# Performance work log

Measured on AMD Instinct MI355X. Metric: run time of the kernel, lower is better.

The kernel has to match this reference:

```python
import jax, jax.numpy as jnp
import numpy as np

B_, N, C = 4096, 49, 384
H = 12
HD = C // H
NW = 64
SCALE = HD ** -0.5


def setup_inputs() -> dict:
    key = jax.random.key(0)
    k_x, k_m, k_w1, k_b1, k_w2, k_b2 = jax.random.split(key, 6)
    x = jax.random.normal(k_x, (B_, N, C), dtype=jnp.float32)
    # shifted-window style additive mask: 0 = allowed, -100 = blocked
    mask = jnp.where(jax.random.uniform(k_m, (NW, N, N)) < 0.5, 0.0, -100.0).astype(jnp.float32)
    w_qkv = jax.random.normal(k_w1, (3 * C, C), dtype=jnp.float32) * (C ** -0.5)
    b_qkv = jax.random.normal(k_b1, (3 * C,), dtype=jnp.float32) * 0.02
    w_proj = jax.random.normal(k_w2, (C, C), dtype=jnp.float32) * (C ** -0.5)
    b_proj = jax.random.normal(k_b2, (C,), dtype=jnp.float32) * 0.02
    return {"x": x, "mask": mask, "w_qkv": w_qkv, "b_qkv": b_qkv,
            "w_proj": w_proj, "b_proj": b_proj}


def reference(x, mask, w_qkv, b_qkv, w_proj, b_proj):
    # qkv projection: (B_, N, 3C)
    qkv = x @ w_qkv.T + b_qkv
    qkv = qkv.reshape(B_, N, 3, H, HD).transpose(2, 0, 3, 1, 4)  # (3, B_, H, N, HD)
    q, k, v = qkv[0], qkv[1], qkv[2]
    q = q * SCALE
    attn = jnp.einsum('bhnd,bhmd->bhnm', q, k)  # (B_, H, N, N)
    # additive shifted-window mask, per-window pattern broadcast over batch & heads
    attn = attn.reshape(B_ // NW, NW, H, N, N) + mask[None, :, None]
    attn = attn.reshape(B_, H, N, N)
    attn = jax.nn.softmax(attn, axis=-1)
    out = jnp.einsum('bhnm,bhmd->bhnd', attn, v)  # (B_, H, N, HD)
    out = out.transpose(0, 2, 1, 3).reshape(B_, N, C)
    return out @ w_proj.T + b_proj
```

## Files before the change

kernel.cpp:

```cpp
#include <hip/hip_runtime.h>
#include <cstdio>
#include <cstdint>


typedef __attribute__((ext_vector_type(8))) short bfrag8;
typedef __attribute__((ext_vector_type(4))) float facc4;
typedef __attribute__((ext_vector_type(16))) float facc16;

#define SCALE_Q 0.17677669529663687f
#define PLANE 6422528ull

__device__ __forceinline__ unsigned short f2bf(float f) {
  unsigned int x = __float_as_uint(f);
  x += 0x7fffu + ((x >> 16) & 1u);
  return (unsigned short)(x >> 16);
}

__device__ __forceinline__ void gload_lds16(const void* g, void* l) {
  __builtin_amdgcn_global_load_lds(
      (const __attribute__((address_space(1))) unsigned int*)g,
      (__attribute__((address_space(3))) unsigned int*)l,
      16, 0, 0);
}

__global__ void __launch_bounds__(256) cvt_bf16_kernel(const float* __restrict__ src,
                                                       unsigned short* __restrict__ dst) {
  size_t i = ((size_t)blockIdx.x * 256u + threadIdx.x) * 4u;
  const float4 v = *(const float4*)(src + i);
  ushort4 o;
  o.x = f2bf(v.x); o.y = f2bf(v.y); o.z = f2bf(v.z); o.w = f2bf(v.w);
  *(ushort4*)(dst + i) = o;
}

__global__ void __launch_bounds__(256) mask_bits_kernel(
    const float* __restrict__ mask, unsigned long long* __restrict__ bits) {
  const int idx = blockIdx.x * 256 + threadIdx.x;
  const int wdw = idx >> 6, m = idx & 63;
  unsigned long long bm = 0ull;
  if (m < 49) {
    const float* mp = mask + (size_t)wdw * 2401 + (size_t)m * 49;
    for (int n = 0; n < 49; ++n)
      if (mp[n] > -50.f) bm |= (1ull << n);
  }
  bits[idx] = bm;
}

__global__ void __launch_bounds__(256) wswz32_kernel(const float* __restrict__ w,
                                                     unsigned short* __restrict__ Bf) {
  const int t = blockIdx.x * 256 + threadIdx.x;
  const int fid = t >> 6, lc = t & 63;
  const int cg = fid / 24, ksl = fid - cg * 24;
  const int col = cg * 32 + (lc & 31);
  const int k = ksl * 16 + (lc >> 5) * 8;
  const float* src = w + (size_t)col * 384 + k;
  unsigned short* dst = Bf + ((size_t)fid << 9) + (lc << 3);
#pragma unroll
  for (int j = 0; j < 8; ++j) dst[j] = f2bf(src[j]);
}

#define LB32(dst, ks_)                                                         \
  {                                                                            \
    _Pragma("unroll") for (int ni = 0; ni < 3; ++ni)                           \
        dst[ni] = *(const bfrag8*)(                                            \
            Bf + ((size_t)((cg0 + ni) * 24 + (ks_)) << 9) + (lane << 3));      \
  }

#define MF32(bb, ks_)                                                          \
  {                                                                            \
    const bfrag8 af0 = *(const bfrag8*)(Ab + ((size_t)(ks_) << 10));           \
    const bfrag8 af1 = *(const bfrag8*)(Ab + ((size_t)(24 + (ks_)) << 10));    \
    _Pragma("unroll") for (int ni = 0; ni < 3; ++ni) {                         \
      acc[0][ni] = __builtin_amdgcn_mfma_f32_32x32x16_bf16(af0, bb[ni],        \
                                                           acc[0][ni], 0, 0, 0);\
      acc[1][ni] = __builtin_amdgcn_mfma_f32_32x32x16_bf16(af1, bb[ni],        \
                                                           acc[1][ni], 0, 0, 0);\
    }                                                                          \
  }

template <int NR, int MODE, int SWZ>
__global__ void __launch_bounds__(512, 1) gemm_32(
    const unsigned short* __restrict__ A, const unsigned short* __restrict__ Bf,
    const float* __restrict__ bias,
    unsigned short* __restrict__ qkv, float* __restrict__ f_out) {
  __shared__ __align__(16) unsigned short Alds[128 * 384];

  int bid = blockIdx.x;
  bid = (bid & 7) * SWZ + (bid >> 3);
  const int tid = threadIdx.x;
  const int lane = tid & 63, w = tid >> 6;
  const int wr = w >> 2, wc = w & 3;
  const int l31 = lane & 31, l5 = lane >> 5;
  const size_t a_row0 = (size_t)bid * 128;

#pragma unroll
  for (int j = 0; j < 12; ++j) {
    const int fid = w + j * 8;
    const int rg = fid / 24, ksl = fid - rg * 24;
    const int row = rg * 32 + l31;
    const int k = ksl * 16 + l5 * 8;
    gload_lds16(A + (a_row0 + row) * 384 + k,
                (char*)Alds + ((w << 10) + (j << 13)));
  }
  __syncthreads();

  const char* Ab = (const char*)Alds + ((size_t)(wr * 48) << 10) + (lane << 4);

  for (int rnd = 0; rnd < NR; ++rnd) {
    const int cg0 = (rnd * 4 + wc) * 3;
    facc16 acc[2][3];
#pragma unroll
    for (int mi = 0; mi < 2; ++mi)
#pragma unroll
      for (int ni = 0; ni < 3; ++ni)
#pragma unroll
        for (int r = 0; r < 16; ++r) acc[mi][ni][r] = 0.f;

    bfrag8 bA[3], bB[3];
    LB32(bA, 0);
    LB32(bB, 1);
#pragma unroll 1
    for (int ks = 0; ks < 24; ks += 2) {
      MF32(bA, ks);
      if (ks + 2 < 24) LB32(bA, ks + 2);
      MF32(bB, ks + 1);
      if (ks + 3 < 24) LB32(bB, ks + 3);
    }

    if (MODE == 0) {
#pragma unroll
      for (int ni = 0; ni < 3; ++ni) {
        const int j0 = (cg0 + ni) * 32;
        const int t = j0 / 384;
        const int rj = j0 - t * 384;
        const int h = rj >> 5;
        unsigned short* pl = qkv + (size_t)(t * 12 + h) * PLANE + l31;
        const float bvv = bias[j0 + l31];
        const float sc = (t == 0) ? SCALE_Q : 1.0f;
#pragma unroll
        for (int mi = 0; mi < 2; ++mi)
#pragma unroll
          for (int r = 0; r < 16; ++r) {
            const size_t m = a_row0 + wr * 64 + mi * 32 +
                             (r & 3) + 8 * (r >> 2) + 4 * l5;
            pl[m * 32] = f2bf((acc[mi][ni][r] + bvv) * sc);
          }
      }
    } else {
#pragma unroll
      for (int ni = 0; ni < 3; ++ni) {
        const int col = (cg0 + ni) * 32 + l31;
        const float bvv = bias[col];
#pragma unroll
        for (int mi = 0; mi < 2; ++mi)
#pragma unroll
          for (int r = 0; r < 16; ++r) {
            const size_t m = a_row0 + wr * 64 + mi * 32 +
                             (r & 3) + 8 * (r >> 2) + 4 * l5;
            f_out[m * 384 + col] = acc[mi][ni][r] + bvv;
          }
      }
    }
  }
}

__global__ void __launch_bounds__(64) attn_kernel(
    const unsigned short* __restrict__ QKV,
    const unsigned long long* __restrict__ mbits,
    unsigned short* __restrict__ Og) {
  __shared__ unsigned short Vt[32 * 64];
  __shared__ unsigned short Ps[64 * 64];

  const int bid = blockIdx.x;
  const int b = bid / 12, h = bid - b * 12;
  const int lane = threadIdx.x;
  const int l15 = lane & 15, l4 = lane >> 4;

  const bfrag8 z8 = {0, 0, 0, 0, 0, 0, 0, 0};
  const facc4 fz = {0.f, 0.f, 0.f, 0.f};

  const size_t wb = (size_t)b * 49 * 32;
  const unsigned short* Qp = QKV + (size_t)h * PLANE + wb;
  const unsigned short* Kp = QKV + (size_t)(12 + h) * PLANE + wb;
  const unsigned short* Vp = QKV + (size_t)(24 + h) * PLANE + wb;

#pragma unroll
  for (int i = 0; i < 4; ++i)
    *(bfrag8*)((char*)Vt + (lane + i * 64) * 16) = z8;

#pragma unroll
  for (int i = 0; i < 4; ++i) {
    const int c = lane + i * 64;
    if (c < 196) {
      const bfrag8 vv = *(const bfrag8*)(Vp + c * 8);
      const int n = c >> 2, cc = c & 3;
      const int d0 = cc * 8;
#pragma unroll
      for (int jj = 0; jj < 8; ++jj) {
        const int d = d0 + jj;
        *(unsigned short*)((char*)Vt + (((d << 7) + (n << 1)) ^ ((d & 7) << 4))) =
            (unsigned short)vv[jj];
      }
    }
  }
  __syncthreads();

  facc4 s[4][4];
  {
    bfrag8 qa[4], kf[4];
#pragma unroll
    for (int mi = 0; mi < 4; ++mi)
      qa[mi] = *(const bfrag8*)((const char*)Qp + (mi * 16 + l15) * 64 + l4 * 16);
#pragma unroll
    for (int ni = 0; ni < 4; ++ni)
      kf[ni] = *(const bfrag8*)((const char*)Kp + (ni * 16 + l15) * 64 + l4 * 16);
#pragma unroll
    for (int mi = 0; mi < 4; ++mi)
#pragma unroll
      for (int ni = 0; ni < 4; ++ni)
        s[mi][ni] = __builtin_amdgcn_mfma_f32_16x16x32_bf16(qa[mi], kf[ni], fz, 0, 0, 0);
  }

  const unsigned long long* mb = mbits + (size_t)(b & 63) * 64;
  float rinv[4][4];
#pragma unroll
  for (int mi = 0; mi < 4; ++mi)
#pragma unroll
    for (int r = 0; r < 4; ++r) {
      const int m = mi * 16 + l4 * 4 + r;
      const unsigned long long mw = mb[m];
      float mx = -1e30f;
      int ok[4];
#pragma unroll
      for (int ni = 0; ni < 4; ++ni) {
        const int n = ni * 16 + l15;
        ok[ni] = (int)((mw >> n) & 1ull);
        const float v = ok[ni] ? s[mi][ni][r] : -1e30f;
        mx = fmaxf(mx, v);
      }
      mx = fmaxf(mx, __shfl_xor(mx, 1));
      mx = fmaxf(mx, __shfl_xor(mx, 2));
      mx = fmaxf(mx, __shfl_xor(mx, 4));
      mx = fmaxf(mx, __shfl_xor(mx, 8));
      float sum = 0.f;
#pragma unroll
      for (int ni = 0; ni < 4; ++ni) {
        const float p = ok[ni] ? __expf(s[mi][ni][r] - mx) : 0.f;
        s[mi][ni][r] = p;
        sum += p;
      }
      sum += __shfl_xor(sum, 1);
      sum += __shfl_xor(sum, 2);
      sum += __shfl_xor(sum, 4);
      sum += __shfl_xor(sum, 8);
      rinv[mi][r] = 1.0f / sum;
#pragma unroll
      for (int ni = 0; ni < 4; ++ni) {
        const int n = ni * 16 + l15;
        *(unsigned short*)((char*)Ps + (((m << 7) + (n << 1)) ^ ((m & 7) << 4))) =
            f2bf(s[mi][ni][r]);
      }
    }
  __syncthreads();

  facc4 o[4][2];
#pragma unroll
  for (int mi = 0; mi < 4; ++mi)
#pragma unroll
    for (int di = 0; di < 2; ++di) o[mi][di] = fz;
#pragma unroll
  for (int kk = 0; kk < 2; ++kk) {
    bfrag8 pa[4], vb[2];
#pragma unroll
    for (int mi = 0; mi < 4; ++mi) {
      const int row = mi * 16 + l15;
      pa[mi] = *(const bfrag8*)((const char*)Ps +
                                (((row << 7) + kk * 64 + (l4 << 4)) ^ ((row & 7) << 4)));
    }
#pragma unroll
    for (int di = 0; di < 2; ++di) {
      const int row = di * 16 + l15;
      vb[di] = *(const bfrag8*)((const char*)Vt +
                                (((row << 7) + kk * 64 + (l4 << 4)) ^ ((row & 7) << 4)));
    }
#pragma unroll
    for (int mi = 0; mi < 4; ++mi)
#pragma unroll
      for (int di = 0; di < 2; ++di)
        o[mi][di] = __builtin_amdgcn_mfma_f32_16x16x32_bf16(pa[mi], vb[di], o[mi][di], 0, 0, 0);
  }

  unsigned short* op = Og + (size_t)b * 18816 + h * 32;
#pragma unroll
  for (int mi = 0; mi < 4; ++mi)
#pragma unroll
    for (int r = 0; r < 4; ++r) {
      const int m = mi * 16 + l4 * 4 + r;
      if (m < 49) {
        const float rs = rinv[mi][r];
#pragma unroll
        for (int di = 0; di < 2; ++di)
          op[(size_t)m * 384 + di * 16 + l15] = f2bf(o[mi][di][r] * rs);
      }
    }
}

extern "C" void kernel_launch(void* const* d_in, const int* in_sizes, int n_in,
                              void* d_out, int out_size, void* d_ws, size_t ws_size,
                              hipStream_t stream) {
  const float* x      = (const float*)d_in[0];
  const float* mask   = (const float*)d_in[1];
  const float* w_qkv  = (const float*)d_in[2];
  const float* b_qkv  = (const float*)d_in[3];
  const float* w_proj = (const float*)d_in[4];
  const float* b_proj = (const float*)d_in[5];
  float* out = (float*)d_out;

  const size_t E = 77070336ull;
  unsigned short* wsu   = (unsigned short*)d_ws;
  unsigned short* qkvp  = wsu;
  unsigned short* o_ws  = wsu + 3 * E;
  unsigned short* xbf   = wsu + 4 * E;
  unsigned short* Bfq   = wsu + 5 * E;
  unsigned short* Bfp   = Bfq + 442368ull;
  unsigned long long* mb = (unsigned long long*)(Bfp + 147456ull);
  const size_t need = (5 * E + 442368ull + 147456ull) * 2ull + 4096ull * 8ull;
  if (ws_size < need) {
    fprintf(stderr, "[WindowAttention] ws too small: need=%zu have=%zu\n",
            (size_t)need, ws_size);
    return;
  }

  cvt_bf16_kernel<<<75264, 256, 0, stream>>>(x, xbf);
  wswz32_kernel<<<216, 256, 0, stream>>>(w_qkv, Bfq);
  wswz32_kernel<<<72, 256, 0, stream>>>(w_proj, Bfp);
  mask_bits_kernel<<<16, 256, 0, stream>>>(mask, mb);

  gemm_32<3, 0, 196><<<1568, 512, 0, stream>>>(xbf, Bfq, b_qkv, qkvp, nullptr);

  attn_kernel<<<49152, 64, 0, stream>>>(qkvp, mb, o_ws);

  gemm_32<1, 1, 196><<<1568, 512, 0, stream>>>(o_ws, Bfp, b_proj, nullptr, out);
}
```

Measured before the change: 696.8 us.

## Fuse fp32-to-bf16 input conversion into QKV GEMM load and triple-buffer B fragments

```diff
diff --git a/kernel.cpp b/kernel.cpp
--- a/kernel.cpp
+++ b/kernel.cpp
@@ -21,15 +21,6 @@
       (const __attribute__((address_space(1))) unsigned int*)g,
       (__attribute__((address_space(3))) unsigned int*)l,
       16, 0, 0);
-}
-
-__global__ void __launch_bounds__(256) cvt_bf16_kernel(const float* __restrict__ src,
-                                                       unsigned short* __restrict__ dst) {
-  size_t i = ((size_t)blockIdx.x * 256u + threadIdx.x) * 4u;
-  const float4 v = *(const float4*)(src + i);
-  ushort4 o;
-  o.x = f2bf(v.x); o.y = f2bf(v.y); o.z = f2bf(v.z); o.w = f2bf(v.w);
-  *(ushort4*)(dst + i) = o;
 }
 
 __global__ void __launch_bounds__(256) mask_bits_kernel(
@@ -79,8 +70,8 @@
 
 template <int NR, int MODE, int SWZ>
 __global__ void __launch_bounds__(512, 1) gemm_32(
-    const unsigned short* __restrict__ A, const unsigned short* __restrict__ Bf,
-    const float* __restrict__ bias,
+    const float* __restrict__ Af32, const unsigned short* __restrict__ Abf,
+    const unsigned short* __restrict__ Bf, const float* __restrict__ bias,
     unsigned short* __restrict__ qkv, float* __restrict__ f_out) {
   __shared__ __align__(16) unsigned short Alds[128 * 384];
 
@@ -92,14 +83,31 @@
   const int l31 = lane & 31, l5 = lane >> 5;
   const size_t a_row0 = (size_t)bid * 128;
 
-#pragma unroll
-  for (int j = 0; j < 12; ++j) {
-    const int fid = w + j * 8;
-    const int rg = fid / 24, ksl = fid - rg * 24;
-    const int row = rg * 32 + l31;
-    const int k = ksl * 16 + l5 * 8;
-    gload_lds16(A + (a_row0 + row) * 384 + k,
-                (char*)Alds + ((w << 10) + (j << 13)));
+  if (MODE == 0) {
+    const int arow = tid >> 2, seg = tid & 3;
+    const float* asrc = Af32 + (a_row0 + arow) * 384 + seg * 96;
+    const int rg = arow >> 5, lifr = arow & 31;
+#pragma unroll
+    for (int j = 0; j < 24; ++j) {
+      const int k0 = seg * 96 + j * 4;
+      const float4 v = *(const float4*)(asrc + j * 4);
+      ushort4 h4;
+      h4.x = f2bf(v.x); h4.y = f2bf(v.y); h4.z = f2bf(v.z); h4.w = f2bf(v.w);
+      const int fid = rg * 24 + (k0 >> 4);
+      const int lif = lifr + ((k0 & 15) >> 3) * 32;
+      *(ushort4*)((char*)Alds + ((size_t)fid << 10) + (lif << 4) +
+                  ((k0 & 7) << 1)) = h4;
+    }
+  } else {
+#pragma unroll
+    for (int j = 0; j < 12; ++j) {
+      const int fid = w + j * 8;
+      const int rg = fid / 24, ksl = fid - rg * 24;
+      const int row = rg * 32 + l31;
+      const int k = ksl * 16 + l5 * 8;
+      gload_lds16(Abf + (a_row0 + row) * 384 + k,
+                  (char*)Alds + ((w << 10) + (j << 13)));
+    }
   }
   __syncthreads();
 
@@ -115,15 +123,18 @@
 #pragma unroll
         for (int r = 0; r < 16; ++r) acc[mi][ni][r] = 0.f;
 
-    bfrag8 bA[3], bB[3];
+    bfrag8 bA[3], bB[3], bC[3];
     LB32(bA, 0);
     LB32(bB, 1);
+    LB32(bC, 2);
 #pragma unroll 1
-    for (int ks = 0; ks < 24; ks += 2) {
+    for (int ks = 0; ks < 24; ks += 3) {
       MF32(bA, ks);
-      if (ks + 2 < 24) LB32(bA, ks + 2);
+      if (ks + 3 < 24) LB32(bA, ks + 3);
       MF32(bB, ks + 1);
-      if (ks + 3 < 24) LB32(bB, ks + 3);
+      if (ks + 4 < 24) LB32(bB, ks + 4);
+      MF32(bC, ks + 2);
+      if (ks + 5 < 24) LB32(bC, ks + 5);
     }
 
     if (MODE == 0) {
@@ -319,25 +330,25 @@
   unsigned short* wsu   = (unsigned short*)d_ws;
   unsigned short* qkvp  = wsu;
   unsigned short* o_ws  = wsu + 3 * E;
-  unsigned short* xbf   = wsu + 4 * E;
-  unsigned short* Bfq   = wsu + 5 * E;
+  unsigned short* Bfq   = wsu + 4 * E;
   unsigned short* Bfp   = Bfq + 442368ull;
   unsigned long long* mb = (unsigned long long*)(Bfp + 147456ull);
-  const size_t need = (5 * E + 442368ull + 147456ull) * 2ull + 4096ull * 8ull;
+  const size_t need = (4 * E + 442368ull + 147456ull) * 2ull + 4096ull * 8ull;
   if (ws_size < need) {
     fprintf(stderr, "[WindowAttention] ws too small: need=%zu have=%zu\n",
             (size_t)need, ws_size);
     return;
   }
 
-  cvt_bf16_kernel<<<75264, 256, 0, stream>>>(x, xbf);
   wswz32_kernel<<<216, 256, 0, stream>>>(w_qkv, Bfq);
   wswz32_kernel<<<72, 256, 0, stream>>>(w_proj, Bfp);
   mask_bits_kernel<<<16, 256, 0, stream>>>(mask, mb);
 
-  gemm_32<3, 0, 196><<<1568, 512, 0, stream>>>(xbf, Bfq, b_qkv, qkvp, nullptr);
+  gemm_32<3, 0, 196><<<1568, 512, 0, stream>>>(x, nullptr, Bfq, b_qkv,
+                                               qkvp, nullptr);
 
   attn_kernel<<<49152, 64, 0, stream>>>(qkvp, mb, o_ws);
 
-  gemm_32<1, 1, 196><<<1568, 512, 0, stream>>>(o_ws, Bfp, b_proj, nullptr, out);
-}
+  gemm_32<1, 1, 196><<<1568, 512, 0, stream>>>(nullptr, o_ws, Bfp, b_proj,
+                                               nullptr, out);
+}
```

Result: faster. 669.8 us (-3.9%).
